# Kernel tuning notes

Hardware: AMD Instinct MI355X
Metric: run time of the kernel (lower is better)

## Reference

```python
import jax, jax.numpy as jnp
import numpy as np

# dims: B batch, T frames, N tokens/frame, C embed, H heads, D=C//H, MEM memory slots
B, T, N, C = 8, 16, 196, 768
H = 8
D = C // H
MEM = 196          # mem_size; with N=196 -> _init_t = 1, M stays == MEM
HID = 4 * C        # mlp_ratio * embed_dim
STD = 0.02


def _mlp(x, w1, b1, w2, b2):
    # timm-style Mlp: fc1 -> GELU -> fc2 (dropout = 0)
    return jax.nn.gelu(x @ w1 + b1, approximate=False) @ w2 + b2


def _ln(x, w, b, eps=1e-5):
    mu = jnp.mean(x, axis=-1, keepdims=True)
    var = jnp.var(x, axis=-1, keepdims=True)
    return (x - mu) * jax.lax.rsqrt(var + eps) * w + b


def setup_inputs() -> dict:
    key = jax.random.key(0)
    ks = jax.random.split(key, 10)
    f32 = jnp.float32
    return {
        "cur_fea": jax.random.normal(ks[0], (B, T, N, C), f32),
        "norm1_w": jnp.ones((C,), f32), "norm1_b": jnp.zeros((C,), f32),
        "norm2_w": jnp.ones((C,), f32), "norm2_b": jnp.zeros((C,), f32),
        # c_func: Mlp(2C -> 4C -> C)
        "c_w1": jax.random.normal(ks[1], (2 * C, HID), f32) * STD, "c_b1": jnp.zeros((HID,), f32),
        "c_w2": jax.random.normal(ks[2], (HID, C), f32) * STD, "c_b2": jnp.zeros((C,), f32),
        # m_func: Mlp(C -> 4C -> C)
        "m_w1": jax.random.normal(ks[3], (C, HID), f32) * STD, "m_b1": jnp.zeros((HID,), f32),
        "m_w2": jax.random.normal(ks[4], (HID, C), f32) * STD, "m_b2": jnp.zeros((C,), f32),
        # post_func: Mlp(C -> 4C -> C)
        "p_w1": jax.random.normal(ks[5], (C, HID), f32) * STD, "p_b1": jnp.zeros((HID,), f32),
        "p_w2": jax.random.normal(ks[6], (HID, C), f32) * STD, "p_b2": jnp.zeros((C,), f32),
        # ProjectDotDistance: per-head q(c_global) . k(mem) * scale -> sigmoid
        "q_w": jax.random.normal(ks[7], (C, C), f32) * STD, "q_b": jnp.zeros((C,), f32),
        "k_w": jax.random.normal(ks[8], (C, C), f32) * STD, "k_b": jnp.zeros((C,), f32),
    }


def reference(cur_fea, norm1_w, norm1_b, norm2_w, norm2_b,
              c_w1, c_b1, c_w2, c_b2, m_w1, m_b1, m_w2, m_b2,
              p_w1, p_b1, p_w2, p_b2, q_w, q_b, k_w, k_b):
    x = _ln(cur_fea, norm1_w, norm1_b)                       # [B,T,N,C]
    # T*N > mem_size, _init_t = MEM // N = 1 -> init memory = frame 0 (no grad, torch.no_grad)
    init_mem = jax.lax.stop_gradient(x[:, 0].reshape(B, MEM, C))
    scale = D ** -0.5

    def step(mem, fea):                                      # mem [B,MEM,C], fea [B,N,C]
        ap = jnp.mean(mem, axis=1, keepdims=True)            # [B,1,C]
        cg = _mlp(jnp.concatenate([fea, jnp.broadcast_to(ap, fea.shape)], axis=-1),
                  c_w1, c_b1, c_w2, c_b2)                    # [B,N,C]
        memh = _mlp(mem, m_w1, m_b1, m_w2, m_b2).reshape(B, MEM, H, D).transpose(0, 2, 1, 3)  # [B,H,M,D]
        q = (cg @ q_w + q_b).reshape(B, N, H, D).transpose(0, 2, 1, 3)    # [B,H,N,D]
        k = (mem @ k_w + k_b).reshape(B, MEM, H, D).transpose(0, 2, 1, 3) # [B,H,M,D]
        o = jax.nn.sigmoid(jnp.einsum('bhnd,bhmd->bhnm', q, k) * scale)   # [B,H,N,M]
        cgh = cg.reshape(B, N, H, D).transpose(0, 2, 1, 3)               # [B,H,N,D]
        c = jnp.einsum('bhnm,bhnd->bmhd', o, cgh).reshape(B, MEM, C)
        c = _mlp(c, p_w1, p_b1, p_w2, p_b2)
        # mean_N((1-o) * broadcast(memh)) == mean_N(1-o) * memh (memh indep of N)
        gate = jnp.mean(1.0 - o, axis=2)                     # [B,H,M]
        og = (gate[..., None] * memh).transpose(0, 2, 1, 3).reshape(B, MEM, C)
        new_mem = _ln(c + og, norm2_w, norm2_b)
        return new_mem, None

    fea_seq = x[:, 1:].transpose(1, 0, 2, 3)                 # [T-1,B,N,C]
    final_mem, _ = jax.lax.scan(step, init_mem, fea_seq)
    return final_mem                                         # [B,MEM,C]
```

## Files before the change

### kernel.cpp

```cpp
#include <hip/hip_runtime.h>
#include <hip/hip_bf16.h>
#include <math.h>

constexpr int B_   = 8;
constexpr int T_   = 16;
constexpr int N_   = 196;
constexpr int C_   = 768;
constexpr int H_   = 8;
constexpr int D_   = 96;
constexpr int M_   = 196;
constexpr int HID_ = 3072;
constexpr int ROWS_ = B_ * N_;
constexpr int MP_   = 1664;

typedef __hip_bfloat16 bf16;
typedef __attribute__((ext_vector_type(8))) short bf16x8;
typedef __attribute__((ext_vector_type(4))) float f32x4;

__device__ __forceinline__ float b2f(bf16 x) { return __bfloat162float(x); }
__device__ __forceinline__ short bf2s(bf16 x) { union { bf16 b; short s; } u; u.b = x; return u.s; }
__device__ __forceinline__ float s2f(short x) { union { bf16 b; short s; } u; u.s = x; return __bfloat162float(u.b); }

#define GL2LDS(g, l) __builtin_amdgcn_global_load_lds( \
    (__attribute__((address_space(1))) void*)(g), \
    (__attribute__((address_space(3))) void*)(l), 16, 0, 0)

__device__ __forceinline__ void hard_barrier() {
    asm volatile("" ::: "memory");
    __builtin_amdgcn_s_barrier();
    asm volatile("" ::: "memory");
}

__device__ __forceinline__ int3 xcd_map() {
    const int gx = gridDim.x, gy = gridDim.y;
    const int nwg = gx * gy * gridDim.z;
    const int lid = blockIdx.x + gx * (blockIdx.y + gy * blockIdx.z);
    const int q = nwg >> 3, r = nwg & 7;
    const int xcd = lid & 7, pos = lid >> 3;
    const int wg = (xcd < r) ? (xcd * (q + 1) + pos)
                             : (r * (q + 1) + (xcd - r) * q + pos);
    int3 c;
    c.x = wg % gx;
    int t = wg / gx;
    c.y = t % gy;
    c.z = t / gy;
    return c;
}

__device__ __forceinline__ float block_reduce_sum256(float v, float* sdata) {
    int tid = threadIdx.x;
    sdata[tid] = v;
    __syncthreads();
    for (int s = 128; s > 0; s >>= 1) {
        if (tid < s) sdata[tid] += sdata[tid + s];
        __syncthreads();
    }
    float r = sdata[0];
    __syncthreads();
    return r;
}

struct TEnt { const float* W; bf16* Wt; int K; int N; int tiles; };
struct TEnts { TEnt e[8]; };

__global__ __launch_bounds__(256) void transpose_all_kernel(TEnts tds)
{
    __shared__ float tile[32][33];
    int local = blockIdx.x;
    int i = 0;
    while (i < 7 && local >= tds.e[i].tiles) { local -= tds.e[i].tiles; ++i; }
    TEnt g = tds.e[i];
    int ntx = g.N / 32;
    int n0 = (local % ntx) * 32, k0 = (local / ntx) * 32;
    int tx = threadIdx.x & 31, ty = threadIdx.x >> 5;
#pragma unroll
    for (int r = 0; r < 32; r += 8)
        tile[ty + r][tx] = g.W[(size_t)(k0 + ty + r) * g.N + n0 + tx];
    __syncthreads();
#pragma unroll
    for (int r = 0; r < 32; r += 8)
        g.Wt[(size_t)(n0 + ty + r) * g.K + k0 + tx] = __float2bfloat16(tile[tx][ty + r]);
}

__global__ __launch_bounds__(256) void cvt_kernel(const float* __restrict__ W,
                                                  bf16* __restrict__ o, int n)
{
    int i = blockIdx.x * 256 + threadIdx.x;
    if (i < n) o[i] = __float2bfloat16(W[i]);
}

__global__ __launch_bounds__(256) void ln_frame_kernel(
    const float* __restrict__ cur, int t,
    const float* __restrict__ w, const float* __restrict__ bia,
    bf16* __restrict__ mem_bf)
{
    __shared__ float sdata[256];
    int row = blockIdx.x;
    int b = row / N_, n = row % N_;
    const float* src = cur + (((size_t)b * T_ + t) * N_ + n) * C_;
    float x[3];
    float sum = 0.f, sumsq = 0.f;
#pragma unroll
    for (int i = 0; i < 3; i++) {
        int c = threadIdx.x + i * 256;
        x[i] = src[c];
        sum += x[i]; sumsq += x[i] * x[i];
    }
    sum = block_reduce_sum256(sum, sdata);
    sumsq = block_reduce_sum256(sumsq, sdata);
    float mu = sum * (1.0f / C_);
    float var = sumsq * (1.0f / C_) - mu * mu;
    float rs = rsqrtf(var + 1e-5f);
#pragma unroll
    for (int i = 0; i < 3; i++) {
        int c = threadIdx.x + i * 256;
        mem_bf[(size_t)row * C_ + c] = __float2bfloat16((x[i] - mu) * rs * w[c] + bia[c]);
    }
}

__global__ __launch_bounds__(256) void ap_partial_kernel(const bf16* __restrict__ mem,
                                                         float* __restrict__ app)
{
    int ch = blockIdx.x, b = blockIdx.y;
    int m0 = ch * 25;
    int m1 = m0 + 25; if (m1 > M_) m1 = M_;
    const bf16* p = mem + (size_t)b * M_ * C_;
#pragma unroll
    for (int i = 0; i < 3; i++) {
        int c = threadIdx.x + i * 256;
        float s = 0.f;
        for (int m = m0; m < m1; m++) s += b2f(p[(size_t)m * C_ + c]);
        app[((size_t)b * 8 + ch) * C_ + c] = s;
    }
}

__global__ __launch_bounds__(256) void build_cat_kernel(
    const float* __restrict__ cur, int t,
    const float* __restrict__ w, const float* __restrict__ bia,
    const float* __restrict__ app, bf16* __restrict__ cat)
{
    __shared__ float sdata[256];
    int row = blockIdx.x;
    int b = row / N_, n = row % N_;
    const float* src = cur + (((size_t)b * T_ + t) * N_ + n) * C_;
    float x[3];
    float sum = 0.f, sumsq = 0.f;
#pragma unroll
    for (int i = 0; i < 3; i++) {
        int c = threadIdx.x + i * 256;
        x[i] = src[c];
        sum += x[i]; sumsq += x[i] * x[i];
    }
    sum = block_reduce_sum256(sum, sdata);
    sumsq = block_reduce_sum256(sumsq, sdata);
    float mu = sum * (1.0f / C_);
    float var = sumsq * (1.0f / C_) - mu * mu;
    float rs = rsqrtf(var + 1e-5f);
    bf16* dstrow = cat + (size_t)row * (2 * C_);
#pragma unroll
    for (int i = 0; i < 3; i++) {
        int c = threadIdx.x + i * 256;
        dstrow[c] = __float2bfloat16((x[i] - mu) * rs * w[c] + bia[c]);
        float apv = 0.f;
#pragma unroll
        for (int j = 0; j < 8; j++) apv += app[((size_t)b * 8 + j) * C_ + c];
        dstrow[C_ + c] = __float2bfloat16(apv * (1.0f / M_));
    }
}

struct GemmDesc {
    const bf16* A; const bf16* W; const float* bias; bf16* out;
    int K; int N; int ymax; int gelu;
};
struct GemmDescs { GemmDesc d[4]; };

template <int BN>
__global__ __launch_bounds__(256) void mfma_gemm_multi(GemmDescs ds)
{
    constexpr int BM = 128;
    constexpr int TI = 4;
    constexpr int TJ = (BN / 2) / 16;
    constexpr int ABYTES = BM * 128;
    constexpr int BBYTES = BN * 128;
    constexpr int AR = ABYTES / 4096;
    constexpr int BR = BBYTES / 4096;
    constexpr int NL = AR + BR;
    __shared__ short As[2 * BM * 64];
    __shared__ short Bs[2 * BN * 64];

    const int3 bc = xcd_map();
    GemmDesc g = ds.d[bc.z];
    if (bc.y >= g.ymax) return;

    int tid = threadIdx.x;
    int wid = tid >> 6;
    int lane = tid & 63;
    int quad = lane >> 4, l15 = lane & 15;
    int row0 = bc.x * BM;
    int col0 = bc.y * BN;
    int wm = (wid >> 1) * 64;
    int wn = (wid & 1) * (BN / 2);

    f32x4 acc[TI][TJ] = {};

    const char* Ab = (const char*)g.A;
    const char* Wb = (const char*)g.W;
    const size_t Kb = (size_t)g.K * 2;
    const int base = wid * 1024;

    auto stage = [&](int k0, int sel) {
        char* Ad = (char*)As + sel * ABYTES;
        char* Bd = (char*)Bs + sel * BBYTES;
#pragma unroll
        for (int r = 0; r < AR; r++) {
            int o = r * 4096 + base + lane * 16;
            int row = o >> 7, cs = (o >> 4) & 7;
            int kc = cs ^ (row & 7);
            GL2LDS(Ab + (size_t)(row0 + row) * Kb + (size_t)k0 * 2 + kc * 16, Ad + o);
        }
#pragma unroll
        for (int r = 0; r < BR; r++) {
            int o = r * 4096 + base + lane * 16;
            int row = o >> 7, cs = (o >> 4) & 7;
            int kc = cs ^ (row & 7);
            GL2LDS(Wb + (size_t)(col0 + row) * Kb + (size_t)k0 * 2 + kc * 16, Bd + o);
        }
    };

    const int nk = g.K / 64;
    stage(0, 0);
    for (int ki = 0; ki < nk; ki++) {
        int sel = ki & 1;
        if (ki + 1 < nk) {
            stage((ki + 1) * 64, sel ^ 1);
            asm volatile("s_waitcnt vmcnt(%0)" :: "n"(NL) : "memory");
        } else {
            asm volatile("s_waitcnt vmcnt(0)" ::: "memory");
        }
        hard_barrier();
        const bf16x8* Av = (const bf16x8*)(As + sel * BM * 64);
        const bf16x8* Bv = (const bf16x8*)(Bs + sel * BN * 64);
        bf16x8 af[TI][2], bfr[TJ][2];
#pragma unroll
        for (int i = 0; i < TI; i++) {
            int r = wm + i * 16 + l15;
#pragma unroll
            for (int hh = 0; hh < 2; hh++)
                af[i][hh] = Av[r * 8 + ((hh * 4 + quad) ^ (r & 7))];
        }
#pragma unroll
        for (int j = 0; j < TJ; j++) {
            int r = wn + j * 16 + l15;
#pragma unroll
            for (int hh = 0; hh < 2; hh++)
                bfr[j][hh] = Bv[r * 8 + ((hh * 4 + quad) ^ (r & 7))];
        }
#pragma unroll
        for (int hh = 0; hh < 2; hh++)
#pragma unroll
            for (int i = 0; i < TI; i++)
#pragma unroll
                for (int j = 0; j < TJ; j++)
                    acc[i][j] = __builtin_amdgcn_mfma_f32_16x16x32_bf16(
                        af[i][hh], bfr[j][hh], acc[i][j], 0, 0, 0);
        hard_barrier();
    }

#pragma unroll
    for (int i = 0; i < TI; i++) {
        int gr = row0 + wm + i * 16 + quad * 4;
#pragma unroll
        for (int j = 0; j < TJ; j++) {
            int gc = col0 + wn + j * 16 + l15;
            float bv = g.bias ? g.bias[gc] : 0.0f;
#pragma unroll
            for (int r = 0; r < 4; r++) {
                float v = acc[i][j][r] + bv;
                if (g.gelu) v = 0.5f * v * (1.0f + erff(v * 0.7071067811865475f));
                g.out[(size_t)(gr + r) * g.N + gc] = __float2bfloat16(v);
            }
        }
    }
}

__global__ __launch_bounds__(256) void mfma_gemm_splitk(
    const bf16* __restrict__ A, const bf16* __restrict__ Wt,
    float* __restrict__ part, int K)
{
    constexpr int BM = 128;
    constexpr int BN = 64;
    constexpr int TI = 4;
    constexpr int TJ = 2;
    constexpr int ABYTES = BM * 128, BBYTES = BN * 128;
    constexpr int AR = 4, BR = 2, NL = 6;
    __shared__ short As[2 * BM * 64];
    __shared__ short Bs[2 * BN * 64];

    const int3 bc = xcd_map();
    int tid = threadIdx.x;
    int wid = tid >> 6;
    int lane = tid & 63;
    int quad = lane >> 4, l15 = lane & 15;
    int row0 = bc.x * BM;
    int col0 = bc.y * BN;
    int wm = (wid >> 1) * 64;
    int wn = (wid & 1) * 32;
    int kh = K >> 1;
    int kbeg = bc.z * kh;

    f32x4 acc[TI][TJ] = {};
    const char* Ab = (const char*)A;
    const char* Wb = (const char*)Wt;
    const size_t Kb = (size_t)K * 2;
    const int base = wid * 1024;

    auto stage = [&](int k0, int sel) {
        char* Ad = (char*)As + sel * ABYTES;
        char* Bd = (char*)Bs + sel * BBYTES;
#pragma unroll
        for (int r = 0; r < AR; r++) {
            int o = r * 4096 + base + lane * 16;
            int row = o >> 7, cs = (o >> 4) & 7;
            int kc = cs ^ (row & 7);
            GL2LDS(Ab + (size_t)(row0 + row) * Kb + (size_t)k0 * 2 + kc * 16, Ad + o);
        }
#pragma unroll
        for (int r = 0; r < BR; r++) {
            int o = r * 4096 + base + lane * 16;
            int row = o >> 7, cs = (o >> 4) & 7;
            int kc = cs ^ (row & 7);
            GL2LDS(Wb + (size_t)(col0 + row) * Kb + (size_t)k0 * 2 + kc * 16, Bd + o);
        }
    };

    const int nk = kh / 64;
    stage(kbeg, 0);
    for (int ki = 0; ki < nk; ki++) {
        int sel = ki & 1;
        if (ki + 1 < nk) {
            stage(kbeg + (ki + 1) * 64, sel ^ 1);
            asm volatile("s_waitcnt vmcnt(%0)" :: "n"(NL) : "memory");
        } else {
            asm volatile("s_waitcnt vmcnt(0)" ::: "memory");
        }
        hard_barrier();
        const bf16x8* Av = (const bf16x8*)(As + sel * BM * 64);
        const bf16x8* Bv = (const bf16x8*)(Bs + sel * BN * 64);
        bf16x8 af[TI][2], bfr[TJ][2];
#pragma unroll
        for (int i = 0; i < TI; i++) {
            int r = wm + i * 16 + l15;
#pragma unroll
            for (int hh = 0; hh < 2; hh++)
                af[i][hh] = Av[r * 8 + ((hh * 4 + quad) ^ (r & 7))];
        }
#pragma unroll
        for (int j = 0; j < TJ; j++) {
            int r = wn + j * 16 + l15;
#pragma unroll
            for (int hh = 0; hh < 2; hh++)
                bfr[j][hh] = Bv[r * 8 + ((hh * 4 + quad) ^ (r & 7))];
        }
#pragma unroll
        for (int hh = 0; hh < 2; hh++)
#pragma unroll
            for (int i = 0; i < TI; i++)
#pragma unroll
                for (int j = 0; j < TJ; j++)
                    acc[i][j] = __builtin_amdgcn_mfma_f32_16x16x32_bf16(
                        af[i][hh], bfr[j][hh], acc[i][j], 0, 0, 0);
        hard_barrier();
    }

    float* outp = part + (size_t)bc.z * MP_ * C_;
#pragma unroll
    for (int i = 0; i < TI; i++) {
        int gr = row0 + wm + i * 16 + quad * 4;
#pragma unroll
        for (int j = 0; j < TJ; j++) {
            int gc = col0 + wn + j * 16 + l15;
#pragma unroll
            for (int r = 0; r < 4; r++)
                outp[(size_t)(gr + r) * C_ + gc] = acc[i][j][r];
        }
    }
}

__global__ __launch_bounds__(256) void b2q_kernel(
    const float* __restrict__ c_b2, const float* __restrict__ q_b,
    const bf16* __restrict__ W2q_t, float* __restrict__ b2q)
{
    __shared__ float sdata[256];
    int n = blockIdx.x;
    const bf16* row = W2q_t + (size_t)n * HID_;
    float s = 0.f;
    for (int j = threadIdx.x; j < HID_; j += 256) s += c_b2[j] * b2f(row[j]);
    s = block_reduce_sum256(s, sdata);
    if (threadIdx.x == 0) b2q[n] = s + q_b[n];
}

__global__ __launch_bounds__(512) void attn_mfma_kernel(
    const bf16* __restrict__ q, const bf16* __restrict__ k,
    const bf16* __restrict__ cg, bf16* __restrict__ cbuf,
    float* __restrict__ gate)
{
    constexpr int KS = 104;
    constexpr int PSS = 40;
    __shared__ short Ks[64 * KS];
    __shared__ short Qs[32 * KS];
    __shared__ short CGt[96 * PSS];
    __shared__ short Ph[64 * PSS];
    __shared__ short Pl[64 * PSS];
    __shared__ float gred[8][64];

    const int3 bc = xcd_map();
    const int mt = bc.x, h = bc.y, b = bc.z;
    const int m0 = (mt < 3) ? mt * 64 : (M_ - 64);
    const int tid = threadIdx.x;
    const int w = tid >> 6, lane = tid & 63;
    const int quad = lane >> 4, l15 = lane & 15;
    const int wm = w >> 1;
    const int wh = w & 1;
    const float scale = 0.10206207261596575f;

    const bf16* qp = q  + (size_t)b * N_ * C_ + h * D_;
    const bf16* kp = k  + (size_t)b * M_ * C_ + h * D_;
    const bf16* cp = cg + (size_t)b * N_ * C_ + h * D_;

    for (int idx = tid; idx < 64 * 12; idx += 512) {
        int r = idx / 12, c = idx % 12;
        *(bf16x8*)(Ks + r * KS + c * 8) =
            *(const bf16x8*)(kp + (size_t)(m0 + r) * C_ + c * 8);
    }

    f32x4 acc[3] = {};
    float gacc = 0.f;

    const bf16x8 ZEROV = {0, 0, 0, 0, 0, 0, 0, 0};
    bf16x8 qv = ZEROV, cgv = ZEROV;
    const bool active = tid < 32 * 12;
    const int qrow = tid / 12, qcol = (tid % 12) * 8;
    const int cgn = tid & 31, cgd = (tid >> 5) * 8;

    auto issue = [&](int n0) {
        if (!active) return;
        int nq = n0 + qrow;
        qv = (nq < N_) ? *(const bf16x8*)(qp + (size_t)nq * C_ + qcol) : ZEROV;
        int nc = n0 + cgn;
        cgv = (nc < N_) ? *(const bf16x8*)(cp + (size_t)nc * C_ + cgd) : ZEROV;
    };
    auto stage = [&]() {
        if (!active) return;
        *(bf16x8*)(Qs + qrow * KS + qcol) = qv;
#pragma unroll
        for (int i = 0; i < 8; i++) CGt[(cgd + i) * PSS + cgn] = cgv[i];
    };

    issue(0);
    for (int nt = 0; nt < 7; nt++) {
        stage();
        __syncthreads();
        if (nt < 6) issue((nt + 1) * 32);

        f32x4 s4 = {};
#pragma unroll
        for (int kk = 0; kk < 3; kk++) {
            bf16x8 af = *(const bf16x8*)(Ks + (wm * 16 + l15) * KS + kk * 32 + quad * 8);
            bf16x8 bq = *(const bf16x8*)(Qs + (wh * 16 + l15) * KS + kk * 32 + quad * 8);
            s4 = __builtin_amdgcn_mfma_f32_16x16x32_bf16(af, bq, s4, 0, 0, 0);
        }
        const int nglob = nt * 32 + wh * 16 + l15;
#pragma unroll
        for (int r = 0; r < 4; r++) {
            float p = (nglob < N_) ? 1.f / (1.f + expf(-s4[r] * scale)) : 0.f;
            bf16 hb = __float2bfloat16(p);
            bf16 lb = __float2bfloat16(p - __bfloat162float(hb));
            int po = (wm * 16 + quad * 4 + r) * PSS + wh * 16 + l15;
            Ph[po] = bf2s(hb);
            Pl[po] = bf2s(lb);
        }
        __syncthreads();

        {
            const short* ph = Ph + lane * PSS + w * 4;
            const short* pl = Pl + lane * PSS + w * 4;
#pragma unroll
            for (int u = 0; u < 4; u++) gacc += s2f(ph[u]) + s2f(pl[u]);
        }
        bf16x8 pa = *(const bf16x8*)(Ph + (wm * 16 + l15) * PSS + quad * 8);
        bf16x8 pb = *(const bf16x8*)(Pl + (wm * 16 + l15) * PSS + quad * 8);
#pragma unroll
        for (int dt = 0; dt < 3; dt++) {
            bf16x8 bcg = *(const bf16x8*)(CGt + (wh * 48 + dt * 16 + l15) * PSS + quad * 8);
            acc[dt] = __builtin_amdgcn_mfma_f32_16x16x32_bf16(pa, bcg, acc[dt], 0, 0, 0);
            acc[dt] = __builtin_amdgcn_mfma_f32_16x16x32_bf16(pb, bcg, acc[dt], 0, 0, 0);
        }
        __syncthreads();
    }

#pragma unroll
    for (int dt = 0; dt < 3; dt++)
#pragma unroll
        for (int r = 0; r < 4; r++) {
            int m = m0 + wm * 16 + quad * 4 + r;
            cbuf[((size_t)b * M_ + m) * C_ + h * D_ + wh * 48 + dt * 16 + l15] =
                __float2bfloat16(acc[dt][r]);
        }
    gred[w][lane] = gacc;
    __syncthreads();
    if (tid < 64) {
        float g = 0.f;
#pragma unroll
        for (int s = 0; s < 8; s++) g += gred[s][tid];
        gate[((size_t)b * H_ + h) * M_ + m0 + tid] = 1.f - g * (1.0f / N_);
    }
}

__global__ __launch_bounds__(256) void final_kernel(
    const float* __restrict__ part, const float* __restrict__ p_b2,
    const float* __restrict__ gate, const bf16* __restrict__ memh,
    const float* __restrict__ w, const float* __restrict__ bia,
    bf16* __restrict__ mem_bf, float* __restrict__ outp)
{
    __shared__ float sdata[256];
    int row = blockIdx.x;
    int b = row / M_, m = row % M_;
    float x[3];
    float sum = 0.f, sumsq = 0.f;
#pragma unroll
    for (int i = 0; i < 3; i++) {
        int c = threadIdx.x + i * 256;
        int h = c / D_;
        float v = part[(size_t)row * C_ + c] + part[(size_t)MP_ * C_ + (size_t)row * C_ + c]
                + p_b2[c]
                + gate[(b * H_ + h) * M_ + m] * b2f(memh[(size_t)row * C_ + c]);
        x[i] = v;
        sum += v; sumsq += v * v;
    }
    sum = block_reduce_sum256(sum, sdata);
    sumsq = block_reduce_sum256(sumsq, sdata);
    float mu = sum * (1.0f / C_);
    float var = sumsq * (1.0f / C_) - mu * mu;
    float rs = rsqrtf(var + 1e-5f);
#pragma unroll
    for (int i = 0; i < 3; i++) {
        int c = threadIdx.x + i * 256;
        float v = (x[i] - mu) * rs * w[c] + bia[c];
        mem_bf[(size_t)row * C_ + c] = __float2bfloat16(v);
        if (outp) outp[(size_t)row * C_ + c] = v;
    }
}

extern "C" void kernel_launch(void* const* d_in, const int* in_sizes, int n_in,
                              void* d_out, int out_size, void* d_ws, size_t ws_size,
                              hipStream_t stream)
{
    const float* cur_fea = (const float*)d_in[0];
    const float* n1w = (const float*)d_in[1];
    const float* n1b = (const float*)d_in[2];
    const float* n2w = (const float*)d_in[3];
    const float* n2b = (const float*)d_in[4];
    const float* c_w1 = (const float*)d_in[5];
    const float* c_b1 = (const float*)d_in[6];
    const float* c_w2 = (const float*)d_in[7];
    const float* c_b2 = (const float*)d_in[8];
    const float* m_w1 = (const float*)d_in[9];
    const float* m_b1 = (const float*)d_in[10];
    const float* m_w2 = (const float*)d_in[11];
    const float* m_b2 = (const float*)d_in[12];
    const float* p_w1 = (const float*)d_in[13];
    const float* p_b1 = (const float*)d_in[14];
    const float* p_w2 = (const float*)d_in[15];
    const float* p_b2 = (const float*)d_in[16];
    const float* q_w = (const float*)d_in[17];
    const float* q_b = (const float*)d_in[18];
    const float* k_w = (const float*)d_in[19];
    const float* k_b = (const float*)d_in[20];

    size_t off = 0;
    char* base = (char*)d_ws;
    auto carve = [&](size_t bytes) -> char* {
        char* r = base + off;
        off += (bytes + 255) & ~(size_t)255;
        return r;
    };
    bf16* cw1t = (bf16*)carve((size_t)HID_ * (2 * C_) * 2);
    bf16* cw2t = (bf16*)carve((size_t)C_ * HID_ * 2);
    bf16* mw1t = (bf16*)carve((size_t)HID_ * C_ * 2);
    bf16* mw2t = (bf16*)carve((size_t)C_ * HID_ * 2);
    bf16* pw1t = (bf16*)carve((size_t)HID_ * C_ * 2);
    bf16* pw2t = (bf16*)carve((size_t)C_ * HID_ * 2);
    bf16* qwt  = (bf16*)carve((size_t)C_ * C_ * 2);
    bf16* kwt  = (bf16*)carve((size_t)C_ * C_ * 2);
    bf16* mem_bf = (bf16*)carve((size_t)MP_ * C_ * 2);
    char* catreg = carve((size_t)MP_ * 2 * C_ * 2);
    bf16* cat = (bf16*)catreg;
    bf16* qb  = (bf16*)catreg;
    bf16* kb  = (bf16*)catreg + (size_t)MP_ * C_;
    bf16* hid_c = (bf16*)carve((size_t)MP_ * HID_ * 2);
    char* hidm_reg = carve((size_t)MP_ * HID_ * 2);
    bf16*  hid_m = (bf16*)hidm_reg;
    float* part  = (float*)hidm_reg;
    bf16* cg    = (bf16*)carve((size_t)MP_ * C_ * 2);
    bf16* cbuf  = (bf16*)carve((size_t)MP_ * C_ * 2);
    bf16* memh  = (bf16*)carve((size_t)MP_ * C_ * 2);
    float* ap   = (float*)carve((size_t)B_ * 8 * C_ * 4);
    float* gateb = (float*)carve((size_t)B_ * H_ * M_ * 4);
    float* b2qb  = (float*)carve((size_t)C_ * 4);
    bf16* W2q_t = (bf16*)carve((size_t)C_ * HID_ * 2);
    const bool fuse_q = (off <= ws_size);

    const dim3 blk(256);

    {
        TEnts tds;
        tds.e[0] = { c_w1, cw1t, 2 * C_, HID_, (HID_ / 32) * ((2 * C_) / 32) };
        tds.e[1] = { c_w2, cw2t, HID_, C_, (C_ / 32) * (HID_ / 32) };
        tds.e[2] = { m_w1, mw1t, C_, HID_, (HID_ / 32) * (C_ / 32) };
        tds.e[3] = { m_w2, mw2t, HID_, C_, (C_ / 32) * (HID_ / 32) };
        tds.e[4] = { p_w1, pw1t, C_, HID_, (HID_ / 32) * (C_ / 32) };
        tds.e[5] = { p_w2, pw2t, HID_, C_, (C_ / 32) * (HID_ / 32) };
        tds.e[6] = { q_w, qwt, C_, C_, (C_ / 32) * (C_ / 32) };
        tds.e[7] = { k_w, kwt, C_, C_, (C_ / 32) * (C_ / 32) };
        int total = 4608 + 2304 * 5 + 576 * 2;
        transpose_all_kernel<<<total, blk, 0, stream>>>(tds);
    }

    if (fuse_q) {
        bf16* cw2nt = hid_c;
        cvt_kernel<<<(HID_ * C_ + 255) / 256, blk, 0, stream>>>(c_w2, cw2nt, HID_ * C_);
        GemmDescs ds;
        ds.d[0] = { qwt, cw2nt, nullptr, W2q_t, C_, HID_, HID_ / 128, 0 };
        ds.d[1] = ds.d[0]; ds.d[2] = ds.d[0]; ds.d[3] = ds.d[0];
        mfma_gemm_multi<128><<<dim3(C_ / 128, HID_ / 128, 1), blk, 0, stream>>>(ds);
        b2q_kernel<<<C_, blk, 0, stream>>>(c_b2, q_b, W2q_t, b2qb);
    }

    ln_frame_kernel<<<ROWS_, blk, 0, stream>>>(cur_fea, 0, n1w, n1b, mem_bf);

    for (int t = 1; t < T_; t++) {
        ap_partial_kernel<<<dim3(8, B_), blk, 0, stream>>>(mem_bf, ap);
        build_cat_kernel<<<ROWS_, blk, 0, stream>>>(cur_fea, t, n1w, n1b, ap, cat);

        {
            GemmDescs ds;
            ds.d[0] = { cat,    cw1t, c_b1, hid_c, 2 * C_, HID_, HID_ / 128, 1 };
            ds.d[1] = { mem_bf, mw1t, m_b1, hid_m, C_,     HID_, HID_ / 128, 1 };
            ds.d[2] = ds.d[0]; ds.d[3] = ds.d[0];
            mfma_gemm_multi<128><<<dim3(MP_ / 128, HID_ / 128, 2), blk, 0, stream>>>(ds);
        }
        {
            GemmDescs ds;
            ds.d[0] = { hid_c,  cw2t, c_b2, cg,   HID_, C_, C_ / 64, 0 };
            ds.d[1] = { hid_m,  mw2t, m_b2, memh, HID_, C_, C_ / 64, 0 };
            ds.d[2] = { mem_bf, kwt,  k_b,  kb,   C_,   C_, C_ / 64, 0 };
            ds.d[3] = { hid_c,  W2q_t, b2qb, qb,  HID_, C_, C_ / 64, 0 };
            mfma_gemm_multi<64><<<dim3(MP_ / 128, C_ / 64, fuse_q ? 4 : 3), blk, 0, stream>>>(ds);
        }
        if (!fuse_q) {
            GemmDescs ds;
            ds.d[0] = { cg, qwt, q_b, qb, C_, C_, C_ / 64, 0 };
            ds.d[1] = ds.d[0]; ds.d[2] = ds.d[0]; ds.d[3] = ds.d[0];
            mfma_gemm_multi<64><<<dim3(MP_ / 128, C_ / 64, 1), blk, 0, stream>>>(ds);
        }
        attn_mfma_kernel<<<dim3(4, H_, B_), dim3(512), 0, stream>>>(qb, kb, cg, cbuf, gateb);
        {
            GemmDescs ds;
            ds.d[0] = { cbuf, pw1t, p_b1, hid_c, C_, HID_, HID_ / 64, 1 };
            ds.d[1] = ds.d[0]; ds.d[2] = ds.d[0]; ds.d[3] = ds.d[0];
            mfma_gemm_multi<64><<<dim3(MP_ / 128, HID_ / 64, 1), blk, 0, stream>>>(ds);
        }
        mfma_gemm_splitk<<<dim3(MP_ / 128, C_ / 64, 2), blk, 0, stream>>>(hid_c, pw2t, part, HID_);
        final_kernel<<<ROWS_, blk, 0, stream>>>(part, p_b2, gateb, memh, n2w, n2b,
                                                mem_bf, (t == T_ - 1) ? (float*)d_out : nullptr);
    }
}
```

Baseline: 3.162 ms.

## Fold broadcast memory-mean half of c_func fc1 into per-batch bias

The second half of the concatenated input to c_func's first layer is the same memory mean broadcast across all tokens of a batch. Its product with the lower half of c_w1 is now computed once per batch as a small matvec (apb_kernel) and added as a per-row bias in the GEMM epilogue, which halves the K dimension of the largest per-step GEMM. The XCD remapping is also rewritten to group workgroups per z-slice and falls back to identity for grids that do not divide evenly. The change adds two small kernel launches per step and a per-element bias lookup with an integer divide in the epilogue.

```diff
diff --git a/kernel.cpp b/kernel.cpp
--- a/kernel.cpp
+++ b/kernel.cpp
@@ -32,19 +32,40 @@
 }
 
 __device__ __forceinline__ int3 xcd_map() {
-    const int gx = gridDim.x, gy = gridDim.y;
-    const int nwg = gx * gy * gridDim.z;
-    const int lid = blockIdx.x + gx * (blockIdx.y + gy * blockIdx.z);
-    const int q = nwg >> 3, r = nwg & 7;
-    const int xcd = lid & 7, pos = lid >> 3;
-    const int wg = (xcd < r) ? (xcd * (q + 1) + pos)
-                             : (r * (q + 1) + (xcd - r) * q + pos);
     int3 c;
-    c.x = wg % gx;
-    int t = wg / gx;
-    c.y = t % gy;
-    c.z = t / gy;
-    return c;
+    c.x = blockIdx.x; c.y = blockIdx.y; c.z = blockIdx.z;
+    const int gx = gridDim.x, gy = gridDim.y, gz = gridDim.z;
+    const int gxy = gx * gy;
+    const int total = gxy * gz;
+    const int r = gxy & 7;
+    const bool ok = ((total & 7) == 0) &&
+                    (r == 0 || (r == 4 && (gz & 1) == 0));
+    if (!ok) return c;
+    const int lid = c.x + gx * (c.y + gy * c.z);
+    const int i = lid & 7;
+    int s = lid >> 3;
+    const int q = gxy >> 3;
+    int z = 0;
+    for (;;) {
+        const int rot = (r != 0 && (z & 1)) ? 4 : 0;
+        const int ex = (r != 0 && (((i + rot) & 7) < r)) ? 1 : 0;
+        const int cz = q + ex;
+        if (s < cz) {
+            const int st = (8 - rot) & 7;
+            int cnt_lt = 0;
+            if (r != 0) {
+                const int hi = st + r;
+                const int lo = (i < hi) ? i : hi;
+                cnt_lt = (lo > st) ? (lo - st) : 0;
+            }
+            const int pz = i * q + cnt_lt + s;
+            c.x = pz % gx;
+            c.y = pz / gx;
+            c.z = z;
+            return c;
+        }
+        s -= cz; z++;
+    }
 }
 
 __device__ __forceinline__ float block_reduce_sum256(float v, float* sdata) {
@@ -61,14 +82,14 @@
 }
 
 struct TEnt { const float* W; bf16* Wt; int K; int N; int tiles; };
-struct TEnts { TEnt e[8]; };
+struct TEnts { TEnt e[9]; };
 
 __global__ __launch_bounds__(256) void transpose_all_kernel(TEnts tds)
 {
     __shared__ float tile[32][33];
     int local = blockIdx.x;
     int i = 0;
-    while (i < 7 && local >= tds.e[i].tiles) { local -= tds.e[i].tiles; ++i; }
+    while (i < 8 && local >= tds.e[i].tiles) { local -= tds.e[i].tiles; ++i; }
     TEnt g = tds.e[i];
     int ntx = g.N / 32;
     int n0 = (local % ntx) * 32, k0 = (local / ntx) * 32;
@@ -92,7 +113,7 @@
 __global__ __launch_bounds__(256) void ln_frame_kernel(
     const float* __restrict__ cur, int t,
     const float* __restrict__ w, const float* __restrict__ bia,
-    bf16* __restrict__ mem_bf)
+    bf16* __restrict__ dst)
 {
     __shared__ float sdata[256];
     int row = blockIdx.x;
@@ -114,7 +135,7 @@
 #pragma unroll
     for (int i = 0; i < 3; i++) {
         int c = threadIdx.x + i * 256;
-        mem_bf[(size_t)row * C_ + c] = __float2bfloat16((x[i] - mu) * rs * w[c] + bia[c]);
+        dst[(size_t)row * C_ + c] = __float2bfloat16((x[i] - mu) * rs * w[c] + bia[c]);
     }
 }
 
@@ -134,42 +155,38 @@
     }
 }
 
-__global__ __launch_bounds__(256) void build_cat_kernel(
-    const float* __restrict__ cur, int t,
-    const float* __restrict__ w, const float* __restrict__ bia,
-    const float* __restrict__ app, bf16* __restrict__ cat)
-{
-    __shared__ float sdata[256];
-    int row = blockIdx.x;
-    int b = row / N_, n = row % N_;
-    const float* src = cur + (((size_t)b * T_ + t) * N_ + n) * C_;
-    float x[3];
-    float sum = 0.f, sumsq = 0.f;
-#pragma unroll
-    for (int i = 0; i < 3; i++) {
-        int c = threadIdx.x + i * 256;
-        x[i] = src[c];
-        sum += x[i]; sumsq += x[i] * x[i];
-    }
-    sum = block_reduce_sum256(sum, sdata);
-    sumsq = block_reduce_sum256(sumsq, sdata);
-    float mu = sum * (1.0f / C_);
-    float var = sumsq * (1.0f / C_) - mu * mu;
-    float rs = rsqrtf(var + 1e-5f);
-    bf16* dstrow = cat + (size_t)row * (2 * C_);
-#pragma unroll
-    for (int i = 0; i < 3; i++) {
-        int c = threadIdx.x + i * 256;
-        dstrow[c] = __float2bfloat16((x[i] - mu) * rs * w[c] + bia[c]);
-        float apv = 0.f;
-#pragma unroll
-        for (int j = 0; j < 8; j++) apv += app[((size_t)b * 8 + j) * C_ + c];
-        dstrow[C_ + c] = __float2bfloat16(apv * (1.0f / M_));
-    }
+__global__ __launch_bounds__(768) void ap_fold_kernel(const float* __restrict__ app,
+                                                      float* __restrict__ apf)
+{
+    int b = blockIdx.x, c = threadIdx.x;
+    float s = 0.f;
+#pragma unroll
+    for (int j = 0; j < 8; j++) s += app[((size_t)b * 8 + j) * C_ + c];
+    apf[(size_t)b * C_ + c] = s * (1.0f / M_);
+}
+
+__global__ __launch_bounds__(256) void apb_kernel(
+    const float* __restrict__ apf, const bf16* __restrict__ cw1b,
+    const float* __restrict__ c_b1, float* __restrict__ apb)
+{
+    int b = blockIdx.y;
+    int hid = blockIdx.x * 128 + (threadIdx.x >> 1);
+    int half = threadIdx.x & 1;
+    const bf16* wr = cw1b + (size_t)hid * C_ + half * 384;
+    const float* ar = apf + (size_t)b * C_ + half * 384;
+    float s = 0.f;
+#pragma unroll 4
+    for (int kk = 0; kk < 384; kk += 8) {
+        bf16x8 wv = *(const bf16x8*)(wr + kk);
+#pragma unroll
+        for (int u = 0; u < 8; u++) s += ar[kk + u] * s2f(wv[u]);
+    }
+    s += __shfl_xor(s, 1);
+    if (half == 0) apb[(size_t)b * HID_ + hid] = s + c_b1[hid];
 }
 
 struct GemmDesc {
-    const bf16* A; const bf16* W; const float* bias; bf16* out;
+    const bf16* A; const bf16* W; const float* bias; const float* bias2; bf16* out;
     int K; int N; int ymax; int gelu;
 };
 struct GemmDescs { GemmDesc d[4]; };
@@ -272,9 +289,14 @@
 #pragma unroll
         for (int j = 0; j < TJ; j++) {
             int gc = col0 + wn + j * 16 + l15;
-            float bv = g.bias ? g.bias[gc] : 0.0f;
+            float bvc = g.bias ? g.bias[gc] : 0.0f;
 #pragma unroll
             for (int r = 0; r < 4; r++) {
+                float bv = bvc;
+                if (g.bias2) {
+                    int bb = (gr + r) / 196; if (bb > 7) bb = 7;
+                    bv = g.bias2[(size_t)bb * g.N + gc];
+                }
                 float v = acc[i][j][r] + bv;
                 if (g.gelu) v = 0.5f * v * (1.0f + erff(v * 0.7071067811865475f));
                 g.out[(size_t)(gr + r) * g.N + gc] = __float2bfloat16(v);
@@ -584,7 +606,8 @@
         off += (bytes + 255) & ~(size_t)255;
         return r;
     };
-    bf16* cw1t = (bf16*)carve((size_t)HID_ * (2 * C_) * 2);
+    bf16* cw1t = (bf16*)carve((size_t)HID_ * C_ * 2);
+    bf16* cw1b = (bf16*)carve((size_t)HID_ * C_ * 2);
     bf16* cw2t = (bf16*)carve((size_t)C_ * HID_ * 2);
     bf16* mw1t = (bf16*)carve((size_t)HID_ * C_ * 2);
     bf16* mw2t = (bf16*)carve((size_t)C_ * HID_ * 2);
@@ -594,7 +617,7 @@
     bf16* kwt  = (bf16*)carve((size_t)C_ * C_ * 2);
     bf16* mem_bf = (bf16*)carve((size_t)MP_ * C_ * 2);
     char* catreg = carve((size_t)MP_ * 2 * C_ * 2);
-    bf16* cat = (bf16*)catreg;
+    bf16* xln = (bf16*)catreg;
     bf16* qb  = (bf16*)catreg;
     bf16* kb  = (bf16*)catreg + (size_t)MP_ * C_;
     bf16* hid_c = (bf16*)carve((size_t)MP_ * HID_ * 2);
@@ -604,7 +627,9 @@
     bf16* cg    = (bf16*)carve((size_t)MP_ * C_ * 2);
     bf16* cbuf  = (bf16*)carve((size_t)MP_ * C_ * 2);
     bf16* memh  = (bf16*)carve((size_t)MP_ * C_ * 2);
-    float* ap   = (float*)carve((size_t)B_ * 8 * C_ * 4);
+    float* app  = (float*)carve((size_t)B_ * 8 * C_ * 4);
+    float* apf  = (float*)carve((size_t)B_ * C_ * 4);
+    float* apbb = (float*)carve((size_t)B_ * HID_ * 4);
     float* gateb = (float*)carve((size_t)B_ * H_ * M_ * 4);
     float* b2qb  = (float*)carve((size_t)C_ * 4);
     bf16* W2q_t = (bf16*)carve((size_t)C_ * HID_ * 2);
@@ -614,15 +639,16 @@
 
     {
         TEnts tds;
-        tds.e[0] = { c_w1, cw1t, 2 * C_, HID_, (HID_ / 32) * ((2 * C_) / 32) };
-        tds.e[1] = { c_w2, cw2t, HID_, C_, (C_ / 32) * (HID_ / 32) };
-        tds.e[2] = { m_w1, mw1t, C_, HID_, (HID_ / 32) * (C_ / 32) };
-        tds.e[3] = { m_w2, mw2t, HID_, C_, (C_ / 32) * (HID_ / 32) };
-        tds.e[4] = { p_w1, pw1t, C_, HID_, (HID_ / 32) * (C_ / 32) };
-        tds.e[5] = { p_w2, pw2t, HID_, C_, (C_ / 32) * (HID_ / 32) };
-        tds.e[6] = { q_w, qwt, C_, C_, (C_ / 32) * (C_ / 32) };
-        tds.e[7] = { k_w, kwt, C_, C_, (C_ / 32) * (C_ / 32) };
-        int total = 4608 + 2304 * 5 + 576 * 2;
+        tds.e[0] = { c_w1,                      cw1t, C_, HID_, (HID_ / 32) * (C_ / 32) };
+        tds.e[1] = { c_w1 + (size_t)C_ * HID_,  cw1b, C_, HID_, (HID_ / 32) * (C_ / 32) };
+        tds.e[2] = { c_w2, cw2t, HID_, C_, (C_ / 32) * (HID_ / 32) };
+        tds.e[3] = { m_w1, mw1t, C_, HID_, (HID_ / 32) * (C_ / 32) };
+        tds.e[4] = { m_w2, mw2t, HID_, C_, (C_ / 32) * (HID_ / 32) };
+        tds.e[5] = { p_w1, pw1t, C_, HID_, (HID_ / 32) * (C_ / 32) };
+        tds.e[6] = { p_w2, pw2t, HID_, C_, (C_ / 32) * (HID_ / 32) };
+        tds.e[7] = { q_w, qwt, C_, C_, (C_ / 32) * (C_ / 32) };
+        tds.e[8] = { k_w, kwt, C_, C_, (C_ / 32) * (C_ / 32) };
+        int total = 2304 * 7 + 576 * 2;
         transpose_all_kernel<<<total, blk, 0, stream>>>(tds);
     }
 
@@ -630,7 +656,7 @@
         bf16* cw2nt = hid_c;
         cvt_kernel<<<(HID_ * C_ + 255) / 256, blk, 0, stream>>>(c_w2, cw2nt, HID_ * C_);
         GemmDescs ds;
-        ds.d[0] = { qwt, cw2nt, nullptr, W2q_t, C_, HID_, HID_ / 128, 0 };
+        ds.d[0] = { qwt, cw2nt, nullptr, nullptr, W2q_t, C_, HID_, HID_ / 128, 0 };
         ds.d[1] = ds.d[0]; ds.d[2] = ds.d[0]; ds.d[3] = ds.d[0];
         mfma_gemm_multi<128><<<dim3(C_ / 128, HID_ / 128, 1), blk, 0, stream>>>(ds);
         b2q_kernel<<<C_, blk, 0, stream>>>(c_b2, q_b, W2q_t, b2qb);
@@ -639,34 +665,36 @@
     ln_frame_kernel<<<ROWS_, blk, 0, stream>>>(cur_fea, 0, n1w, n1b, mem_bf);
 
     for (int t = 1; t < T_; t++) {
-        ap_partial_kernel<<<dim3(8, B_), blk, 0, stream>>>(mem_bf, ap);
-        build_cat_kernel<<<ROWS_, blk, 0, stream>>>(cur_fea, t, n1w, n1b, ap, cat);
+        ap_partial_kernel<<<dim3(8, B_), blk, 0, stream>>>(mem_bf, app);
+        ap_fold_kernel<<<B_, 768, 0, stream>>>(app, apf);
+        apb_kernel<<<dim3(HID_ / 128, B_), blk, 0, stream>>>(apf, cw1b, c_b1, apbb);
+        ln_frame_kernel<<<ROWS_, blk, 0, stream>>>(cur_fea, t, n1w, n1b, xln);
 
         {
             GemmDescs ds;
-            ds.d[0] = { cat,    cw1t, c_b1, hid_c, 2 * C_, HID_, HID_ / 128, 1 };
-            ds.d[1] = { mem_bf, mw1t, m_b1, hid_m, C_,     HID_, HID_ / 128, 1 };
+            ds.d[0] = { xln,    cw1t, nullptr, apbb,   hid_c, C_, HID_, HID_ / 128, 1 };
+            ds.d[1] = { mem_bf, mw1t, m_b1,    nullptr, hid_m, C_, HID_, HID_ / 128, 1 };
             ds.d[2] = ds.d[0]; ds.d[3] = ds.d[0];
             mfma_gemm_multi<128><<<dim3(MP_ / 128, HID_ / 128, 2), blk, 0, stream>>>(ds);
         }
         {
             GemmDescs ds;
-            ds.d[0] = { hid_c,  cw2t, c_b2, cg,   HID_, C_, C_ / 64, 0 };
-            ds.d[1] = { hid_m,  mw2t, m_b2, memh, HID_, C_, C_ / 64, 0 };
-            ds.d[2] = { mem_bf, kwt,  k_b,  kb,   C_,   C_, C_ / 64, 0 };
-            ds.d[3] = { hid_c,  W2q_t, b2qb, qb,  HID_, C_, C_ / 64, 0 };
+            ds.d[0] = { hid_c,  cw2t,  c_b2, nullptr, cg,   HID_, C_, C_ / 64, 0 };
+            ds.d[1] = { hid_m,  mw2t,  m_b2, nullptr, memh, HID_, C_, C_ / 64, 0 };
+            ds.d[2] = { mem_bf, kwt,   k_b,  nullptr, kb,   C_,   C_, C_ / 64, 0 };
+            ds.d[3] = { hid_c,  W2q_t, b2qb, nullptr, qb,   HID_, C_, C_ / 64, 0 };
             mfma_gemm_multi<64><<<dim3(MP_ / 128, C_ / 64, fuse_q ? 4 : 3), blk, 0, stream>>>(ds);
         }
         if (!fuse_q) {
             GemmDescs ds;
-            ds.d[0] = { cg, qwt, q_b, qb, C_, C_, C_ / 64, 0 };
+            ds.d[0] = { cg, qwt, q_b, nullptr, qb, C_, C_, C_ / 64, 0 };
             ds.d[1] = ds.d[0]; ds.d[2] = ds.d[0]; ds.d[3] = ds.d[0];
             mfma_gemm_multi<64><<<dim3(MP_ / 128, C_ / 64, 1), blk, 0, stream>>>(ds);
         }
         attn_mfma_kernel<<<dim3(4, H_, B_), dim3(512), 0, stream>>>(qb, kb, cg, cbuf, gateb);
         {
             GemmDescs ds;
-            ds.d[0] = { cbuf, pw1t, p_b1, hid_c, C_, HID_, HID_ / 64, 1 };
+            ds.d[0] = { cbuf, pw1t, p_b1, nullptr, hid_c, C_, HID_, HID_ / 64, 1 };
             ds.d[1] = ds.d[0]; ds.d[2] = ds.d[0]; ds.d[3] = ds.d[0];
             mfma_gemm_multi<64><<<dim3(MP_ / 128, HID_ / 64, 1), blk, 0, stream>>>(ds);
         }
```

New measurement: 3.753 ms. 18.7% more time.
